# Kernel tuning notes

Measured on AMD Instinct MI355X. Metric: run time of the kernel, lower is better.

Reference implementation:

```python
import jax, jax.numpy as jnp
import numpy as np

GAMMA = 1.4
N_PTS, N_IC, HID = 32768, 16384, 128


def _mlp(layers, p):
    # tanh MLP; layers = list of (W, b), last layer linear
    h = p
    for W, b in layers[:-1]:
        h = jnp.tanh(h @ W + b)
    W, b = layers[-1]
    return h @ W + b


def setup_inputs() -> dict:
    key = jax.random.key(0)
    ks = jax.random.split(key, 16)
    d = {
        "x_train": jax.random.uniform(ks[0], (N_PTS, 3), jnp.float32),
        "x_initial": jax.random.uniform(ks[1], (N_IC, 3), jnp.float32),
        "ic": jax.random.uniform(ks[2], (4, 4), jnp.float32),
    }
    def lin(k, fi, fo):
        return jax.random.normal(k, (fi, fo), jnp.float32) * np.float32(np.sqrt(1.0 / fi))
    dims_m = [(3, HID), (HID, HID), (HID, HID), (HID, 4)]
    dims_n = [(3, HID), (HID, HID), (HID, HID), (HID, 1)]
    for i, (fi, fo) in enumerate(dims_m):
        d[f"mw{i}"] = lin(ks[3 + i], fi, fo)
        d[f"mb{i}"] = jnp.zeros((fo,), jnp.float32)
    for i, (fi, fo) in enumerate(dims_n):
        d[f"nw{i}"] = lin(ks[8 + i], fi, fo)
        d[f"nb{i}"] = jnp.zeros((fo,), jnp.float32)
    return d


def _loss(x_train, x_initial, ic,
          mw0, mb0, mw1, mb1, mw2, mb2, mw3, mb3,
          nw0, nb0, nw1, nb1, nw2, nb2, nw3, nb3):
    layers_m = [(mw0, mb0), (mw1, mb1), (mw2, mb2), (mw3, mb3)]
    layers_n = [(nw0, nb0), (nw1, nb1), (nw2, nb2), (nw3, nb3)]

    def prim(p):  # p: (3,) = (x, y, t)
        o = _mlp(layers_m, p)
        rho, pr, u, v = o[0], o[1], o[2], o[3]
        E = pr / (GAMMA - 1.0) + 0.5 * rho * (u * u + v * v)
        return rho, pr, u, v, E

    def Ufn(p):  # conserved state U1..U4
        rho, pr, u, v, E = prim(p)
        return jnp.stack([rho, rho * u, rho * v, E])

    def quant(p):  # [U1..U4, f1..f4, g1..g4]
        rho, pr, u, v, E = prim(p)
        U = jnp.stack([rho, rho * u, rho * v, E])
        f = jnp.stack([rho * u, rho * u * u + pr, rho * u * v, u * (E + pr)])
        g = jnp.stack([rho * v, rho * u * v, rho * v * v + pr, v * (E + pr)])
        return jnp.concatenate([U, f, g])

    # one fused forward-mode Jacobian sweep replaces 20 torch autograd.grad calls
    J = jax.vmap(jax.jacfwd(quant))(x_train)            # (N, 12, 3)
    Hs = jax.vmap(jax.jacfwd(jax.jacfwd(Ufn)))(x_train)  # (N, 4, 3, 3)

    mu = 0.01 * jnp.squeeze(_mlp(layers_n, x_train), -1) ** 2  # (N,)
    lap = Hs[:, :, 0, 0] + Hs[:, :, 1, 1]               # U_xx + U_yy, (N, 4)
    # res_i = U_i_t + f_i_x + g_i_y - mu * (U_i_xx + U_i_yy)
    res = J[:, 0:4, 2] + J[:, 4:8, 0] + J[:, 8:12, 1] - mu[:, None] * lap
    r = jnp.mean(res ** 2, axis=0)                      # (4,) -> r1..r4

    # initial-condition quadrant loss (masked means, jit-safe)
    pred = _mlp(layers_m, x_initial)                    # (Ni, 4)
    xl = x_initial[:, 0] < 0.5
    xr = x_initial[:, 0] > 0.5
    yt = x_initial[:, 1] > 0.5
    yb = x_initial[:, 1] < 0.5
    perm = jnp.array([0, 3, 1, 2])  # ic columns -> [rho, p, u, v] target order
    init_loss = jnp.float32(0.0)
    for row, mask in ((1, xl & yt), (3, xr & yt), (0, xl & yb), (2, xr & yb)):
        tgt = ic[row][perm]                             # (4,)
        m = mask.astype(pred.dtype)
        denom = jnp.maximum(jnp.sum(m), 1.0)
        init_loss = init_loss + jnp.sum(m[:, None] * (pred - tgt) ** 2) / denom

    return jnp.sum(r) + 10.0 * init_loss + 0.1 * jnp.mean(mu ** 2)


def reference(x_train, x_initial, ic,
              mw0, mb0, mw1, mb1, mw2, mb2, mw3, mb3,
              nw0, nb0, nw1, nb1, nw2, nb2, nw3, nb3):
    return _loss(x_train, x_initial, ic,
                 mw0, mb0, mw1, mb1, mw2, mb2, mw3, mb3,
                 nw0, nb0, nw1, nb1, nw2, nb2, nw3, nb3)
```

## Files before the change

kernel.cpp:

```cpp
#include <hip/hip_runtime.h>

#define NPTS 32768
#define NIC  16384
#define GRID 1024
#define BLK  256
#define NW   4

typedef __attribute__((ext_vector_type(8))) _Float16 f16x8;
typedef __attribute__((ext_vector_type(4))) float f32x4;

#define SWZ(e, r) ((e) ^ (((r) & 7) << 3))
#define MFMA16 __builtin_amdgcn_mfma_f32_16x16x32_f16

__device__ __forceinline__ float tanh_fast(float x) {
    float e = __expf(2.0f * x);
    return 1.0f - 2.0f / (e + 1.0f);
}

__device__ __forceinline__ float wave_allsum(float v) {
#pragma unroll
    for (int off = 32; off > 0; off >>= 1) v += __shfl_xor(v, off, 64);
    return v;
}

__device__ __forceinline__ unsigned short f2hb(float x) {
    return __builtin_bit_cast(unsigned short, (_Float16)x);
}
__device__ __forceinline__ uint2 pack4h(float a, float b, float c, float d) {
    return make_uint2((unsigned)f2hb(a) | ((unsigned)f2hb(b) << 16),
                      (unsigned)f2hb(c) | ((unsigned)f2hb(d) << 16));
}

__global__ __launch_bounds__(512) void k_prep(
    const float* __restrict__ mw1, const float* __restrict__ mw2,
    const float* __restrict__ nw1, const float* __restrict__ nw2,
    const float* __restrict__ mw3,
    unsigned short* __restrict__ wt1, unsigned short* __restrict__ wt2,
    unsigned short* __restrict__ nt1, unsigned short* __restrict__ nt2,
    unsigned short* __restrict__ w3t) {
    const int tid = threadIdx.x;
    const int bk = blockIdx.x;
    if (bk == 4) {
        for (int i = tid; i < 2048; i += 512) w3t[i] = 0;
        __syncthreads();
        if (tid < 512) {
            const int j = tid & 127, k = tid >> 7;
            w3t[k * 128 + SWZ(j, k)] = f2hb(mw3[j * 4 + k]);
        }
        return;
    }
    const float* src = (bk == 0) ? mw1 : (bk == 1) ? mw2 : (bk == 2) ? nw1 : nw2;
    unsigned short* dst = (bk == 0) ? wt1 : (bk == 1) ? wt2 : (bk == 2) ? nt1 : nt2;
    __shared__ float sM[128 * 129];
#pragma unroll
    for (int k = 0; k < 32; k++) {
        const int idx = tid + k * 512;
        const int j = idx >> 7, n = idx & 127;
        sM[n * 129 + j] = src[idx];
    }
    __syncthreads();
#pragma unroll
    for (int k = 0; k < 32; k++) {
        const int d = tid + k * 512;
        const int n = d >> 7, js = d & 127;
        const int j = js ^ ((n & 7) << 3);
        dst[d] = f2hb(sM[n * 129 + j]);
    }
}

__device__ __forceinline__ void load_aw(f16x8 (&aW)[2][4],
                                        const unsigned short* __restrict__ w,
                                        int arow0, int arow1, int g, int l15) {
#pragma unroll
    for (int ks = 0; ks < 4; ks++) {
        const int ee = SWZ(ks * 32 + g * 8, l15);
        aW[0][ks] = *(const f16x8*)&w[arow0 + ee];
        aW[1][ks] = *(const f16x8*)&w[arow1 + ee];
    }
}

template <int PT>
__device__ __forceinline__ void hidden_val(const f16x8 (&aW)[2][4], _Float16* sHv,
                                           const float* bias, int wv, int g, int l15) {
    f32x4 acc[2][PT];
#pragma unroll
    for (int rr = 0; rr < 2; rr++)
#pragma unroll
        for (int pt = 0; pt < PT; pt++) acc[rr][pt] = (f32x4){0.f, 0.f, 0.f, 0.f};
#pragma unroll
    for (int ks = 0; ks < 4; ks++) {
        const int ee = SWZ(ks * 32 + g * 8, l15);
#pragma unroll
        for (int pt = 0; pt < PT; pt++) {
            const f16x8 Bv = *(const f16x8*)&sHv[(pt * 16 + l15) * 128 + ee];
            acc[0][pt] = MFMA16(aW[0][ks], Bv, acc[0][pt], 0, 0, 0);
            acc[1][pt] = MFMA16(aW[1][ks], Bv, acc[1][pt], 0, 0, 0);
        }
    }
    __syncthreads();
    float hv[2][PT][4];
#pragma unroll
    for (int rr = 0; rr < 2; rr++)
#pragma unroll
        for (int pt = 0; pt < PT; pt++)
#pragma unroll
            for (int r = 0; r < 4; r++) {
                const int n = wv * 32 + rr * 16 + g * 4 + r;
                hv[rr][pt][r] = tanh_fast(acc[rr][pt][r] + bias[n]);
            }
#pragma unroll
    for (int rr = 0; rr < 2; rr++)
#pragma unroll
        for (int pt = 0; pt < PT; pt++) {
            const int row = pt * 16 + l15;
            *(uint2*)&sHv[row * 128 + SWZ(wv * 32 + rr * 16 + g * 4, row)] =
                pack4h(hv[rr][pt][0], hv[rr][pt][1], hv[rr][pt][2], hv[rr][pt][3]);
        }
}

__device__ __forceinline__ void hidden_res(const f16x8 (&aW)[2][4], _Float16* sH6,
                                           const float* bias, int wv, int g, int l15) {
    f32x4 acc[2][6];
#pragma unroll
    for (int rr = 0; rr < 2; rr++)
#pragma unroll
        for (int c = 0; c < 6; c++) acc[rr][c] = (f32x4){0.f, 0.f, 0.f, 0.f};
#pragma unroll
    for (int ks = 0; ks < 4; ks++) {
        const int ee = SWZ(ks * 32 + g * 8, l15);
#pragma unroll
        for (int c = 0; c < 6; c++) {
            const f16x8 Bv = *(const f16x8*)&sH6[c * 2048 + l15 * 128 + ee];
            acc[0][c] = MFMA16(aW[0][ks], Bv, acc[0][c], 0, 0, 0);
            acc[1][c] = MFMA16(aW[1][ks], Bv, acc[1][c], 0, 0, 0);
        }
    }
    __syncthreads();
    float ch[2][6][4];
#pragma unroll
    for (int rr = 0; rr < 2; rr++)
#pragma unroll
        for (int r = 0; r < 4; r++) {
            const int n = wv * 32 + rr * 16 + g * 4 + r;
            const float z0 = acc[rr][0][r] + bias[n];
            const float a = tanh_fast(z0);
            const float s = 1.f - a * a;
            const float zx = acc[rr][1][r], zy = acc[rr][2][r];
            ch[rr][0][r] = a;
            ch[rr][1][r] = s * zx;
            ch[rr][2][r] = s * zy;
            ch[rr][3][r] = s * acc[rr][3][r];
            ch[rr][4][r] = s * acc[rr][4][r] - 2.f * a * s * zx * zx;
            ch[rr][5][r] = s * acc[rr][5][r] - 2.f * a * s * zy * zy;
        }
#pragma unroll
    for (int rr = 0; rr < 2; rr++) {
        const int eo = l15 * 128 + SWZ(wv * 32 + rr * 16 + g * 4, l15);
#pragma unroll
        for (int c = 0; c < 6; c++)
            *(uint2*)&sH6[c * 2048 + eo] =
                pack4h(ch[rr][c][0], ch[rr][c][1], ch[rr][c][2], ch[rr][c][3]);
    }
}

__global__ __launch_bounds__(BLK) void k_fused(
    const float* __restrict__ xtr, const float* __restrict__ xin,
    const float* __restrict__ icg,
    const float* __restrict__ mw0, const float* __restrict__ mb0,
    const float* __restrict__ mb1, const float* __restrict__ mb2,
    const float* __restrict__ mb3,
    const float* __restrict__ nw0, const float* __restrict__ nb0,
    const float* __restrict__ nb1, const float* __restrict__ nb2,
    const float* __restrict__ nw3, const float* __restrict__ nb3,
    const unsigned short* __restrict__ wt1, const unsigned short* __restrict__ wt2,
    const unsigned short* __restrict__ nt1, const unsigned short* __restrict__ nt2,
    const unsigned short* __restrict__ w3t,
    float* __restrict__ resPart, float* __restrict__ muPart,
    float* __restrict__ icPart) {
    __shared__ __align__(16) _Float16 sH[6 * 2048];
    __shared__ __align__(16) _Float16 sA[2048];
    __shared__ __align__(16) float sW0[2][512];
    __shared__ __align__(16) float sO[384];
    __shared__ float sB[520];
    __shared__ float sMu[32];
    __shared__ float sTq[16];
    __shared__ float sRed[NW][8];

    const int tid = threadIdx.x;
    const int lane = tid & 63, wv = tid >> 6;
    const int g = lane >> 4, l15 = lane & 15;
    const int p16 = tid & 15, chunk = tid >> 4;
    const int arow0 = (wv * 32 + l15) * 128;
    const int arow1 = (wv * 32 + 16 + l15) * 128;

    f16x8 aW[2][4];
    load_aw(aW, nt1, arow0, arow1, g, l15);

    if (tid < 128) { sB[tid] = mb1[tid]; sB[260 + tid] = nb1[tid]; }
    else           { sB[tid] = mb2[tid - 128]; sB[260 + tid] = nb2[tid - 128]; }
    if (tid < 4) sB[256 + tid] = mb3[tid];
    if (tid == 4) sB[516] = nb3[0];
    if (tid < 16) {
        const int k = tid & 3, q = tid >> 2;
        const int row = (q == 0) ? 1 : ((q == 1) ? 3 : ((q == 2) ? 0 : 2));
        const int pc = (k == 0) ? 0 : ((k == 1) ? 3 : ((k == 2) ? 1 : 2));
        sTq[q * 4 + k] = icg[row * 4 + pc];
    }
    for (int i = tid; i < 512; i += BLK) {
        sW0[0][i] = (i < 384) ? nw0[i] : nb0[i - 384];
        sW0[1][i] = (i < 384) ? mw0[i] : mb0[i - 384];
    }
    for (int i = tid; i < 2048; i += BLK) sA[i] = (_Float16)0.f;
    if (tid < 128) sA[tid] = (_Float16)nw3[tid];
    __syncthreads();

    float accMu2 = 0.f;
    {
        const int pt0 = blockIdx.x * 32;
        const int ee0 = SWZ(chunk * 8, p16);
        const float* w0 = &sW0[0][0];
#pragma unroll
        for (int pp = 0; pp < 2; pp++) {
            const int p = pt0 + pp * 16 + p16;
            const float x = xtr[p * 3 + 0], y = xtr[p * 3 + 1], t = xtr[p * 3 + 2];
            float hv[8];
#pragma unroll
            for (int j = 0; j < 8; j++) {
                const int n = chunk * 8 + j;
                hv[j] = tanh_fast(fmaf(w0[n], x, fmaf(w0[128 + n], y,
                                       fmaf(w0[256 + n], t, w0[384 + n]))));
            }
            const uint2 lo = pack4h(hv[0], hv[1], hv[2], hv[3]);
            const uint2 hi = pack4h(hv[4], hv[5], hv[6], hv[7]);
            *(uint4*)&sH[(pp * 16 + p16) * 128 + ee0] = make_uint4(lo.x, lo.y, hi.x, hi.y);
        }
        __syncthreads();
        hidden_val<2>(aW, sH, &sB[260], wv, g, l15);
        load_aw(aW, nt2, arow0, arow1, g, l15);
        __syncthreads();
        hidden_val<2>(aW, sH, &sB[388], wv, g, l15);
        __syncthreads();
        if (wv < 2) {
            f32x4 a4 = (f32x4){0.f, 0.f, 0.f, 0.f};
#pragma unroll
            for (int ks = 0; ks < 4; ks++) {
                const int ee = SWZ(ks * 32 + g * 8, l15);
                const f16x8 Af = *(const f16x8*)&sA[l15 * 128 + ee];
                const f16x8 Bv = *(const f16x8*)&sH[(wv * 16 + l15) * 128 + ee];
                a4 = MFMA16(Af, Bv, a4, 0, 0, 0);
            }
            if (g == 0) {
                const float o = a4[0] + sB[516];
                const float muv = 0.01f * o * o;
                sMu[wv * 16 + l15] = muv;
                accMu2 += muv * muv;
            }
        }
        __syncthreads();
    }
    accMu2 = wave_allsum(accMu2);
    if (lane == 0) sRed[wv][0] = accMu2;
    __syncthreads();
    if (tid == 0)
        muPart[blockIdx.x] = sRed[0][0] + sRed[1][0] + sRed[2][0] + sRed[3][0];

    ((uint4*)sA)[tid] = ((const uint4*)w3t)[tid];
    load_aw(aW, wt1, arow0, arow1, g, l15);

    {
        const int pt0 = blockIdx.x * 16;
        const int ee0 = SWZ(chunk * 8, p16);
        const float* w0 = &sW0[1][0];
        {
            const int p = pt0 + p16;
            const float x = xin[p * 3 + 0], y = xin[p * 3 + 1], t = xin[p * 3 + 2];
            float hv[8];
#pragma unroll
            for (int j = 0; j < 8; j++) {
                const int n = chunk * 8 + j;
                hv[j] = tanh_fast(fmaf(w0[n], x, fmaf(w0[128 + n], y,
                                       fmaf(w0[256 + n], t, w0[384 + n]))));
            }
            const uint2 lo = pack4h(hv[0], hv[1], hv[2], hv[3]);
            const uint2 hi = pack4h(hv[4], hv[5], hv[6], hv[7]);
            *(uint4*)&sH[p16 * 128 + ee0] = make_uint4(lo.x, lo.y, hi.x, hi.y);
        }
        __syncthreads();
        hidden_val<1>(aW, sH, &sB[0], wv, g, l15);
        load_aw(aW, wt2, arow0, arow1, g, l15);
        __syncthreads();
        hidden_val<1>(aW, sH, &sB[128], wv, g, l15);
        __syncthreads();
        float qs[4] = {0, 0, 0, 0}, qc[4] = {0, 0, 0, 0};
        if (wv == 0) {
            f32x4 a4 = (f32x4){0.f, 0.f, 0.f, 0.f};
#pragma unroll
            for (int ks = 0; ks < 4; ks++) {
                const int ee = SWZ(ks * 32 + g * 8, l15);
                const f16x8 Af = *(const f16x8*)&sA[l15 * 128 + ee];
                const f16x8 Bv = *(const f16x8*)&sH[l15 * 128 + ee];
                a4 = MFMA16(Af, Bv, a4, 0, 0, 0);
            }
            if (g == 0) {
                const int p = pt0 + l15;
                const float o0 = a4[0] + sB[256];
                const float o1 = a4[1] + sB[257];
                const float o2 = a4[2] + sB[258];
                const float o3 = a4[3] + sB[259];
                const float x = xin[p * 3 + 0];
                const float y = xin[p * 3 + 1];
                int quad = -1;
                if (x < 0.5f && y > 0.5f) quad = 0;
                else if (x > 0.5f && y > 0.5f) quad = 1;
                else if (x < 0.5f && y < 0.5f) quad = 2;
                else if (x > 0.5f && y < 0.5f) quad = 3;
                if (quad >= 0) {
                    const float d0 = o0 - sTq[quad * 4 + 0];
                    const float d1 = o1 - sTq[quad * 4 + 1];
                    const float d2 = o2 - sTq[quad * 4 + 2];
                    const float d3 = o3 - sTq[quad * 4 + 3];
                    const float ss = d0 * d0 + d1 * d1 + d2 * d2 + d3 * d3;
#pragma unroll
                    for (int qq = 0; qq < 4; qq++) {
                        qs[qq] += (quad == qq) ? ss : 0.f;
                        qc[qq] += (quad == qq) ? 1.f : 0.f;
                    }
                }
            }
        }
        __syncthreads();
#pragma unroll
        for (int qq = 0; qq < 4; qq++) {
            qs[qq] = wave_allsum(qs[qq]);
            qc[qq] = wave_allsum(qc[qq]);
        }
        if (lane == 0) {
#pragma unroll
            for (int qq = 0; qq < 4; qq++) { sRed[wv][qq] = qs[qq]; sRed[wv][4 + qq] = qc[qq]; }
        }
        __syncthreads();
        if (tid == 0) {
#pragma unroll
            for (int q = 0; q < 8; q++)
                icPart[blockIdx.x * 8 + q] =
                    sRed[0][q] + sRed[1][q] + sRed[2][q] + sRed[3][q];
        }
        __syncthreads();
    }

    float racc0 = 0.f, racc1 = 0.f, racc2 = 0.f, racc3 = 0.f;
    const int base = blockIdx.x * 32;
    for (int b = 0; b < 2; b++) {
        const int pt0 = base + b * 16;
        load_aw(aW, wt1, arow0, arow1, g, l15);
        {
            const int p = pt0 + p16;
            const float x = xtr[p * 3 + 0], y = xtr[p * 3 + 1], t = xtr[p * 3 + 2];
            const float* w0 = &sW0[1][0];
            float ch[6][8];
#pragma unroll
            for (int j = 0; j < 8; j++) {
                const int n = chunk * 8 + j;
                const float wx = w0[n], wy = w0[128 + n], wz = w0[256 + n];
                const float z = fmaf(wx, x, fmaf(wy, y, fmaf(wz, t, w0[384 + n])));
                const float a = tanh_fast(z);
                const float s = 1.f - a * a;
                ch[0][j] = a;
                ch[1][j] = s * wx;
                ch[2][j] = s * wy;
                ch[3][j] = s * wz;
                ch[4][j] = -2.f * a * s * wx * wx;
                ch[5][j] = -2.f * a * s * wy * wy;
            }
            const int off = p16 * 128 + SWZ(chunk * 8, p16);
#pragma unroll
            for (int c = 0; c < 6; c++) {
                const uint2 lo = pack4h(ch[c][0], ch[c][1], ch[c][2], ch[c][3]);
                const uint2 hi = pack4h(ch[c][4], ch[c][5], ch[c][6], ch[c][7]);
                *(uint4*)&sH[c * 2048 + off] = make_uint4(lo.x, lo.y, hi.x, hi.y);
            }
        }
        __syncthreads();
        hidden_res(aW, sH, &sB[0], wv, g, l15);
        load_aw(aW, wt2, arow0, arow1, g, l15);
        __syncthreads();
        hidden_res(aW, sH, &sB[128], wv, g, l15);
        __syncthreads();
#pragma unroll
        for (int tt = 0; tt < 2; tt++) {
            const int c = wv + tt * 4;
            if (c < 6) {
                f32x4 a4 = (f32x4){0.f, 0.f, 0.f, 0.f};
#pragma unroll
                for (int ks = 0; ks < 4; ks++) {
                    const int ee = SWZ(ks * 32 + g * 8, l15);
                    const f16x8 Af = *(const f16x8*)&sA[l15 * 128 + ee];
                    const f16x8 Bf = *(const f16x8*)&sH[c * 2048 + l15 * 128 + ee];
                    a4 = MFMA16(Af, Bf, a4, 0, 0, 0);
                }
                if (g == 0) {
                    float4 o = make_float4(a4[0], a4[1], a4[2], a4[3]);
                    if (c == 0) { o.x += sB[256]; o.y += sB[257]; o.z += sB[258]; o.w += sB[259]; }
                    *(float4*)&sO[(c * 16 + l15) * 4] = o;
                }
            }
        }
        __syncthreads();
        if (wv == 0) {
            const int pp = lane & 15;
            const float m = sMu[b * 16 + pp];
            float oq[4][6];
#pragma unroll
            for (int c = 0; c < 6; c++) {
                const float4 o = *(const float4*)&sO[(c * 16 + pp) * 4];
                oq[0][c] = o.x; oq[1][c] = o.y; oq[2][c] = o.z; oq[3][c] = o.w;
            }
            const float rho = oq[0][0], rho_x = oq[0][1], rho_y = oq[0][2],
                        rho_t = oq[0][3], rho_xx = oq[0][4], rho_yy = oq[0][5];
            const float pr = oq[1][0], pr_x = oq[1][1], pr_y = oq[1][2],
                        pr_t = oq[1][3], pr_xx = oq[1][4], pr_yy = oq[1][5];
            const float u = oq[2][0], u_x = oq[2][1], u_y = oq[2][2],
                        u_t = oq[2][3], u_xx = oq[2][4], u_yy = oq[2][5];
            const float v = oq[3][0], v_x = oq[3][1], v_y = oq[3][2],
                        v_t = oq[3][3], v_xx = oq[3][4], v_yy = oq[3][5];

            const float ig1 = 2.5f;
            const float ke = 0.5f * (u * u + v * v);
            const float E = pr * ig1 + rho * ke;
            const float d_x = u * u_x + v * v_x;
            const float d_y = u * u_y + v * v_y;
            const float d_t = u * u_t + v * v_t;
            const float E_x = pr_x * ig1 + rho_x * ke + rho * d_x;
            const float E_y = pr_y * ig1 + rho_y * ke + rho * d_y;
            const float E_t = pr_t * ig1 + rho_t * ke + rho * d_t;
            const float E_xx = pr_xx * ig1 + rho_xx * ke + 2.f * rho_x * d_x +
                               rho * (u_x * u_x + u * u_xx + v_x * v_x + v * v_xx);
            const float E_yy = pr_yy * ig1 + rho_yy * ke + 2.f * rho_y * d_y +
                               rho * (u_y * u_y + u * u_yy + v_y * v_y + v * v_yy);

            const float r1 = rho_t + (rho_x * u + rho * u_x) + (rho_y * v + rho * v_y)
                           - m * (rho_xx + rho_yy);
            const float r2 = (rho_t * u + rho * u_t)
                           + (rho_x * u * u + 2.f * rho * u * u_x + pr_x)
                           + (rho_y * u * v + rho * u_y * v + rho * u * v_y)
                           - m * ((rho_xx * u + 2.f * rho_x * u_x + rho * u_xx)
                                + (rho_yy * u + 2.f * rho_y * u_y + rho * u_yy));
            const float r3 = (rho_t * v + rho * v_t)
                           + (rho_x * u * v + rho * u_x * v + rho * u * v_x)
                           + (rho_y * v * v + 2.f * rho * v * v_y + pr_y)
                           - m * ((rho_xx * v + 2.f * rho_x * v_x + rho * v_xx)
                                + (rho_yy * v + 2.f * rho_y * v_y + rho * v_yy));
            const float r4 = E_t
                           + (u_x * (E + pr) + u * (E_x + pr_x))
                           + (v_y * (E + pr) + v * (E_y + pr_y))
                           - m * (E_xx + E_yy);
            if (lane < 16) {
                racc0 += r1 * r1; racc1 += r2 * r2;
                racc2 += r3 * r3; racc3 += r4 * r4;
            }
        }
        __syncthreads();
    }

    if (wv == 0) {
        racc0 = wave_allsum(racc0);
        racc1 = wave_allsum(racc1);
        racc2 = wave_allsum(racc2);
        racc3 = wave_allsum(racc3);
        if (lane == 0) {
            resPart[blockIdx.x * 4 + 0] = racc0;
            resPart[blockIdx.x * 4 + 1] = racc1;
            resPart[blockIdx.x * 4 + 2] = racc2;
            resPart[blockIdx.x * 4 + 3] = racc3;
        }
    }
}

__global__ void k_fin(const float* __restrict__ resPart, const float* __restrict__ muPart,
                      const float* __restrict__ icPart, float* __restrict__ out) {
    const int lane = threadIdx.x;
    float r[4] = {0, 0, 0, 0};
    float m2 = 0.f;
    float qs[4] = {0, 0, 0, 0}, qc[4] = {0, 0, 0, 0};
    for (int b = lane; b < GRID; b += 64) {
#pragma unroll
        for (int i = 0; i < 4; i++) r[i] += resPart[b * 4 + i];
        m2 += muPart[b];
#pragma unroll
        for (int q = 0; q < 4; q++) {
            qs[q] += icPart[b * 8 + q];
            qc[q] += icPart[b * 8 + 4 + q];
        }
    }
#pragma unroll
    for (int i = 0; i < 4; i++) r[i] = wave_allsum(r[i]);
    m2 = wave_allsum(m2);
#pragma unroll
    for (int q = 0; q < 4; q++) { qs[q] = wave_allsum(qs[q]); qc[q] = wave_allsum(qc[q]); }
    if (lane == 0) {
        const float sumr = (r[0] + r[1] + r[2] + r[3]) / (float)NPTS;
        float init_loss = 0.f;
#pragma unroll
        for (int q = 0; q < 4; q++) init_loss += qs[q] / fmaxf(qc[q], 1.f);
        out[0] = sumr + 10.f * init_loss + 0.1f * (m2 / (float)NPTS);
    }
}

extern "C" void kernel_launch(void* const* d_in, const int* in_sizes, int n_in,
                              void* d_out, int out_size, void* d_ws, size_t ws_size,
                              hipStream_t stream) {
    const float* xtr = (const float*)d_in[0];
    const float* xin = (const float*)d_in[1];
    const float* icg = (const float*)d_in[2];
    const float* mw0 = (const float*)d_in[3];
    const float* mb0 = (const float*)d_in[4];
    const float* mw1 = (const float*)d_in[5];
    const float* mb1 = (const float*)d_in[6];
    const float* mw2 = (const float*)d_in[7];
    const float* mb2 = (const float*)d_in[8];
    const float* mw3 = (const float*)d_in[9];
    const float* mb3 = (const float*)d_in[10];
    const float* nw0 = (const float*)d_in[11];
    const float* nb0 = (const float*)d_in[12];
    const float* nw1 = (const float*)d_in[13];
    const float* nb1 = (const float*)d_in[14];
    const float* nw2 = (const float*)d_in[15];
    const float* nb2 = (const float*)d_in[16];
    const float* nw3 = (const float*)d_in[17];
    const float* nb3 = (const float*)d_in[18];

    float* wsf = (float*)d_ws;
    float* resPart = wsf;
    float* muPart = wsf + 4096;
    float* icPart = wsf + 5120;
    unsigned short* wt1 = (unsigned short*)(wsf + 13312);
    unsigned short* wt2 = wt1 + 16384;
    unsigned short* nt1 = wt2 + 16384;
    unsigned short* nt2 = nt1 + 16384;
    unsigned short* w3t = nt2 + 16384;

    k_prep<<<5, 512, 0, stream>>>(mw1, mw2, nw1, nw2, mw3, wt1, wt2, nt1, nt2, w3t);
    k_fused<<<GRID, BLK, 0, stream>>>(xtr, xin, icg,
                                      mw0, mb0, mb1, mb2, mb3,
                                      nw0, nb0, nb1, nb2, nw3, nb3,
                                      wt1, wt2, nt1, nt2, w3t,
                                      resPart, muPart, icPart);
    k_fin<<<1, 64, 0, stream>>>(resPart, muPart, icPart, (float*)d_out);
}
```

Baseline: 62.66 us.

## Split IC loss into separate blocks and fuse final reduction via atomic counter

The initial-condition forward pass moves out of every main block into 256 dedicated blocks, each handling 64 points with full 4-wave MMA use. Before, each of the 1024 blocks processed 16 IC points using only one wave. The k_fin launch is removed: the last block to finish, detected with an atomic counter reset in k_prep, performs the final reduction. This removes one kernel launch and gives better wave utilisation for the IC work, at the cost of a larger grid, some load imbalance between the two block types, and atomic/fence overhead.

```diff
diff --git a/kernel.cpp b/kernel.cpp
--- a/kernel.cpp
+++ b/kernel.cpp
@@ -2,7 +2,9 @@
 
 #define NPTS 32768
 #define NIC  16384
-#define GRID 1024
+#define GRID_MAIN 1024
+#define GRID_IC   256
+#define GRID_TOT  1280
 #define BLK  256
 #define NW   4
 
@@ -37,10 +39,11 @@
     const float* __restrict__ mw3,
     unsigned short* __restrict__ wt1, unsigned short* __restrict__ wt2,
     unsigned short* __restrict__ nt1, unsigned short* __restrict__ nt2,
-    unsigned short* __restrict__ w3t) {
+    unsigned short* __restrict__ w3t, unsigned int* __restrict__ doneCnt) {
     const int tid = threadIdx.x;
     const int bk = blockIdx.x;
     if (bk == 4) {
+        if (tid == 0) doneCnt[0] = 0u;
         for (int i = tid; i < 2048; i += 512) w3t[i] = 0;
         __syncthreads();
         if (tid < 512) {
@@ -176,7 +179,8 @@
     const unsigned short* __restrict__ nt1, const unsigned short* __restrict__ nt2,
     const unsigned short* __restrict__ w3t,
     float* __restrict__ resPart, float* __restrict__ muPart,
-    float* __restrict__ icPart) {
+    float* __restrict__ icPart, unsigned int* __restrict__ doneCnt,
+    float* __restrict__ out) {
     __shared__ __align__(16) _Float16 sH[6 * 2048];
     __shared__ __align__(16) _Float16 sA[2048];
     __shared__ __align__(16) float sW0[2][512];
@@ -185,6 +189,7 @@
     __shared__ float sMu[32];
     __shared__ float sTq[16];
     __shared__ float sRed[NW][8];
+    __shared__ int sFlag;
 
     const int tid = threadIdx.x;
     const int lane = tid & 63, wv = tid >> 6;
@@ -194,35 +199,222 @@
     const int arow1 = (wv * 32 + 16 + l15) * 128;
 
     f16x8 aW[2][4];
-    load_aw(aW, nt1, arow0, arow1, g, l15);
-
-    if (tid < 128) { sB[tid] = mb1[tid]; sB[260 + tid] = nb1[tid]; }
-    else           { sB[tid] = mb2[tid - 128]; sB[260 + tid] = nb2[tid - 128]; }
-    if (tid < 4) sB[256 + tid] = mb3[tid];
-    if (tid == 4) sB[516] = nb3[0];
-    if (tid < 16) {
-        const int k = tid & 3, q = tid >> 2;
-        const int row = (q == 0) ? 1 : ((q == 1) ? 3 : ((q == 2) ? 0 : 2));
-        const int pc = (k == 0) ? 0 : ((k == 1) ? 3 : ((k == 2) ? 1 : 2));
-        sTq[q * 4 + k] = icg[row * 4 + pc];
-    }
-    for (int i = tid; i < 512; i += BLK) {
-        sW0[0][i] = (i < 384) ? nw0[i] : nb0[i - 384];
-        sW0[1][i] = (i < 384) ? mw0[i] : mb0[i - 384];
-    }
-    for (int i = tid; i < 2048; i += BLK) sA[i] = (_Float16)0.f;
-    if (tid < 128) sA[tid] = (_Float16)nw3[tid];
-    __syncthreads();
-
-    float accMu2 = 0.f;
-    {
-        const int pt0 = blockIdx.x * 32;
+
+    if (blockIdx.x < GRID_MAIN) {
+        load_aw(aW, nt1, arow0, arow1, g, l15);
+        if (tid < 128) { sB[tid] = mb1[tid]; sB[260 + tid] = nb1[tid]; }
+        else           { sB[tid] = mb2[tid - 128]; sB[260 + tid] = nb2[tid - 128]; }
+        if (tid < 4) sB[256 + tid] = mb3[tid];
+        if (tid == 4) sB[516] = nb3[0];
+        for (int i = tid; i < 512; i += BLK) {
+            sW0[0][i] = (i < 384) ? nw0[i] : nb0[i - 384];
+            sW0[1][i] = (i < 384) ? mw0[i] : mb0[i - 384];
+        }
+        for (int i = tid; i < 2048; i += BLK) sA[i] = (_Float16)0.f;
+        if (tid < 128) sA[tid] = (_Float16)nw3[tid];
+        __syncthreads();
+
+        float accMu2 = 0.f;
+        {
+            const int pt0 = blockIdx.x * 32;
+            const int ee0 = SWZ(chunk * 8, p16);
+            const float* w0 = &sW0[0][0];
+#pragma unroll
+            for (int pp = 0; pp < 2; pp++) {
+                const int p = pt0 + pp * 16 + p16;
+                const float x = xtr[p * 3 + 0], y = xtr[p * 3 + 1], t = xtr[p * 3 + 2];
+                float hv[8];
+#pragma unroll
+                for (int j = 0; j < 8; j++) {
+                    const int n = chunk * 8 + j;
+                    hv[j] = tanh_fast(fmaf(w0[n], x, fmaf(w0[128 + n], y,
+                                           fmaf(w0[256 + n], t, w0[384 + n]))));
+                }
+                const uint2 lo = pack4h(hv[0], hv[1], hv[2], hv[3]);
+                const uint2 hi = pack4h(hv[4], hv[5], hv[6], hv[7]);
+                *(uint4*)&sH[(pp * 16 + p16) * 128 + ee0] = make_uint4(lo.x, lo.y, hi.x, hi.y);
+            }
+            __syncthreads();
+            hidden_val<2>(aW, sH, &sB[260], wv, g, l15);
+            load_aw(aW, nt2, arow0, arow1, g, l15);
+            __syncthreads();
+            hidden_val<2>(aW, sH, &sB[388], wv, g, l15);
+            __syncthreads();
+            if (wv < 2) {
+                f32x4 a4 = (f32x4){0.f, 0.f, 0.f, 0.f};
+#pragma unroll
+                for (int ks = 0; ks < 4; ks++) {
+                    const int ee = SWZ(ks * 32 + g * 8, l15);
+                    const f16x8 Af = *(const f16x8*)&sA[l15 * 128 + ee];
+                    const f16x8 Bv = *(const f16x8*)&sH[(wv * 16 + l15) * 128 + ee];
+                    a4 = MFMA16(Af, Bv, a4, 0, 0, 0);
+                }
+                if (g == 0) {
+                    const float o = a4[0] + sB[516];
+                    const float muv = 0.01f * o * o;
+                    sMu[wv * 16 + l15] = muv;
+                    accMu2 += muv * muv;
+                }
+            }
+            __syncthreads();
+        }
+        accMu2 = wave_allsum(accMu2);
+        if (lane == 0) sRed[wv][0] = accMu2;
+        __syncthreads();
+        if (tid == 0)
+            muPart[blockIdx.x] = sRed[0][0] + sRed[1][0] + sRed[2][0] + sRed[3][0];
+
+        ((uint4*)sA)[tid] = ((const uint4*)w3t)[tid];
+
+        float racc0 = 0.f, racc1 = 0.f, racc2 = 0.f, racc3 = 0.f;
+        const int base = blockIdx.x * 32;
+        for (int b = 0; b < 2; b++) {
+            const int pt0 = base + b * 16;
+            load_aw(aW, wt1, arow0, arow1, g, l15);
+            {
+                const int p = pt0 + p16;
+                const float x = xtr[p * 3 + 0], y = xtr[p * 3 + 1], t = xtr[p * 3 + 2];
+                const float* w0 = &sW0[1][0];
+                float ch[6][8];
+#pragma unroll
+                for (int j = 0; j < 8; j++) {
+                    const int n = chunk * 8 + j;
+                    const float wx = w0[n], wy = w0[128 + n], wz = w0[256 + n];
+                    const float z = fmaf(wx, x, fmaf(wy, y, fmaf(wz, t, w0[384 + n])));
+                    const float a = tanh_fast(z);
+                    const float s = 1.f - a * a;
+                    ch[0][j] = a;
+                    ch[1][j] = s * wx;
+                    ch[2][j] = s * wy;
+                    ch[3][j] = s * wz;
+                    ch[4][j] = -2.f * a * s * wx * wx;
+                    ch[5][j] = -2.f * a * s * wy * wy;
+                }
+                const int off = p16 * 128 + SWZ(chunk * 8, p16);
+#pragma unroll
+                for (int c = 0; c < 6; c++) {
+                    const uint2 lo = pack4h(ch[c][0], ch[c][1], ch[c][2], ch[c][3]);
+                    const uint2 hi = pack4h(ch[c][4], ch[c][5], ch[c][6], ch[c][7]);
+                    *(uint4*)&sH[c * 2048 + off] = make_uint4(lo.x, lo.y, hi.x, hi.y);
+                }
+            }
+            __syncthreads();
+            hidden_res(aW, sH, &sB[0], wv, g, l15);
+            load_aw(aW, wt2, arow0, arow1, g, l15);
+            __syncthreads();
+            hidden_res(aW, sH, &sB[128], wv, g, l15);
+            __syncthreads();
+#pragma unroll
+            for (int tt = 0; tt < 2; tt++) {
+                const int c = wv + tt * 4;
+                if (c < 6) {
+                    f32x4 a4 = (f32x4){0.f, 0.f, 0.f, 0.f};
+#pragma unroll
+                    for (int ks = 0; ks < 4; ks++) {
+                        const int ee = SWZ(ks * 32 + g * 8, l15);
+                        const f16x8 Af = *(const f16x8*)&sA[l15 * 128 + ee];
+                        const f16x8 Bf = *(const f16x8*)&sH[c * 2048 + l15 * 128 + ee];
+                        a4 = MFMA16(Af, Bf, a4, 0, 0, 0);
+                    }
+                    if (g == 0) {
+                        float4 o = make_float4(a4[0], a4[1], a4[2], a4[3]);
+                        if (c == 0) { o.x += sB[256]; o.y += sB[257]; o.z += sB[258]; o.w += sB[259]; }
+                        *(float4*)&sO[(c * 16 + l15) * 4] = o;
+                    }
+                }
+            }
+            __syncthreads();
+            if (wv == 0) {
+                const int pp = lane & 15;
+                const float m = sMu[b * 16 + pp];
+                float oq[4][6];
+#pragma unroll
+                for (int c = 0; c < 6; c++) {
+                    const float4 o = *(const float4*)&sO[(c * 16 + pp) * 4];
+                    oq[0][c] = o.x; oq[1][c] = o.y; oq[2][c] = o.z; oq[3][c] = o.w;
+                }
+                const float rho = oq[0][0], rho_x = oq[0][1], rho_y = oq[0][2],
+                            rho_t = oq[0][3], rho_xx = oq[0][4], rho_yy = oq[0][5];
+                const float pr = oq[1][0], pr_x = oq[1][1], pr_y = oq[1][2],
+                            pr_t = oq[1][3], pr_xx = oq[1][4], pr_yy = oq[1][5];
+                const float u = oq[2][0], u_x = oq[2][1], u_y = oq[2][2],
+                            u_t = oq[2][3], u_xx = oq[2][4], u_yy = oq[2][5];
+                const float v = oq[3][0], v_x = oq[3][1], v_y = oq[3][2],
+                            v_t = oq[3][3], v_xx = oq[3][4], v_yy = oq[3][5];
+
+                const float ig1 = 2.5f;
+                const float ke = 0.5f * (u * u + v * v);
+                const float E = pr * ig1 + rho * ke;
+                const float d_x = u * u_x + v * v_x;
+                const float d_y = u * u_y + v * v_y;
+                const float d_t = u * u_t + v * v_t;
+                const float E_x = pr_x * ig1 + rho_x * ke + rho * d_x;
+                const float E_y = pr_y * ig1 + rho_y * ke + rho * d_y;
+                const float E_t = pr_t * ig1 + rho_t * ke + rho * d_t;
+                const float E_xx = pr_xx * ig1 + rho_xx * ke + 2.f * rho_x * d_x +
+                                   rho * (u_x * u_x + u * u_xx + v_x * v_x + v * v_xx);
+                const float E_yy = pr_yy * ig1 + rho_yy * ke + 2.f * rho_y * d_y +
+                                   rho * (u_y * u_y + u * u_yy + v_y * v_y + v * v_yy);
+
+                const float r1 = rho_t + (rho_x * u + rho * u_x) + (rho_y * v + rho * v_y)
+                               - m * (rho_xx + rho_yy);
+                const float r2 = (rho_t * u + rho * u_t)
+                               + (rho_x * u * u + 2.f * rho * u * u_x + pr_x)
+                               + (rho_y * u * v + rho * u_y * v + rho * u * v_y)
+                               - m * ((rho_xx * u + 2.f * rho_x * u_x + rho * u_xx)
+                                    + (rho_yy * u + 2.f * rho_y * u_y + rho * u_yy));
+                const float r3 = (rho_t * v + rho * v_t)
+                               + (rho_x * u * v + rho * u_x * v + rho * u * v_x)
+                               + (rho_y * v * v + 2.f * rho * v * v_y + pr_y)
+                               - m * ((rho_xx * v + 2.f * rho_x * v_x + rho * v_xx)
+                                    + (rho_yy * v + 2.f * rho_y * v_y + rho * v_yy));
+                const float r4 = E_t
+                               + (u_x * (E + pr) + u * (E_x + pr_x))
+                               + (v_y * (E + pr) + v * (E_y + pr_y))
+                               - m * (E_xx + E_yy);
+                if (lane < 16) {
+                    racc0 += r1 * r1; racc1 += r2 * r2;
+                    racc2 += r3 * r3; racc3 += r4 * r4;
+                }
+            }
+            __syncthreads();
+        }
+        if (wv == 0) {
+            racc0 = wave_allsum(racc0);
+            racc1 = wave_allsum(racc1);
+            racc2 = wave_allsum(racc2);
+            racc3 = wave_allsum(racc3);
+            if (lane == 0) {
+                resPart[blockIdx.x * 4 + 0] = racc0;
+                resPart[blockIdx.x * 4 + 1] = racc1;
+                resPart[blockIdx.x * 4 + 2] = racc2;
+                resPart[blockIdx.x * 4 + 3] = racc3;
+            }
+        }
+    } else {
+        const int bid2 = blockIdx.x - GRID_MAIN;
+        load_aw(aW, wt1, arow0, arow1, g, l15);
+        if (tid < 128) { sB[tid] = mb1[tid]; }
+        else           { sB[tid] = mb2[tid - 128]; }
+        if (tid < 4) sB[256 + tid] = mb3[tid];
+        if (tid < 16) {
+            const int k = tid & 3, q = tid >> 2;
+            const int row = (q == 0) ? 1 : ((q == 1) ? 3 : ((q == 2) ? 0 : 2));
+            const int pc = (k == 0) ? 0 : ((k == 1) ? 3 : ((k == 2) ? 1 : 2));
+            sTq[q * 4 + k] = icg[row * 4 + pc];
+        }
+        for (int i = tid; i < 512; i += BLK)
+            sW0[1][i] = (i < 384) ? mw0[i] : mb0[i - 384];
+        ((uint4*)sA)[tid] = ((const uint4*)w3t)[tid];
+        __syncthreads();
+
+        const int pt0 = bid2 * 64;
         const int ee0 = SWZ(chunk * 8, p16);
-        const float* w0 = &sW0[0][0];
-#pragma unroll
-        for (int pp = 0; pp < 2; pp++) {
+        const float* w0 = &sW0[1][0];
+#pragma unroll
+        for (int pp = 0; pp < 4; pp++) {
             const int p = pt0 + pp * 16 + p16;
-            const float x = xtr[p * 3 + 0], y = xtr[p * 3 + 1], t = xtr[p * 3 + 2];
+            const float x = xin[p * 3 + 0], y = xin[p * 3 + 1], t = xin[p * 3 + 2];
             float hv[8];
 #pragma unroll
             for (int j = 0; j < 8; j++) {
@@ -235,12 +427,13 @@
             *(uint4*)&sH[(pp * 16 + p16) * 128 + ee0] = make_uint4(lo.x, lo.y, hi.x, hi.y);
         }
         __syncthreads();
-        hidden_val<2>(aW, sH, &sB[260], wv, g, l15);
-        load_aw(aW, nt2, arow0, arow1, g, l15);
-        __syncthreads();
-        hidden_val<2>(aW, sH, &sB[388], wv, g, l15);
-        __syncthreads();
-        if (wv < 2) {
+        hidden_val<4>(aW, sH, &sB[0], wv, g, l15);
+        load_aw(aW, wt2, arow0, arow1, g, l15);
+        __syncthreads();
+        hidden_val<4>(aW, sH, &sB[128], wv, g, l15);
+        __syncthreads();
+        float qs[4] = {0, 0, 0, 0}, qc[4] = {0, 0, 0, 0};
+        {
             f32x4 a4 = (f32x4){0.f, 0.f, 0.f, 0.f};
 #pragma unroll
             for (int ks = 0; ks < 4; ks++) {
@@ -250,59 +443,7 @@
                 a4 = MFMA16(Af, Bv, a4, 0, 0, 0);
             }
             if (g == 0) {
-                const float o = a4[0] + sB[516];
-                const float muv = 0.01f * o * o;
-                sMu[wv * 16 + l15] = muv;
-                accMu2 += muv * muv;
-            }
-        }
-        __syncthreads();
-    }
-    accMu2 = wave_allsum(accMu2);
-    if (lane == 0) sRed[wv][0] = accMu2;
-    __syncthreads();
-    if (tid == 0)
-        muPart[blockIdx.x] = sRed[0][0] + sRed[1][0] + sRed[2][0] + sRed[3][0];
-
-    ((uint4*)sA)[tid] = ((const uint4*)w3t)[tid];
-    load_aw(aW, wt1, arow0, arow1, g, l15);
-
-    {
-        const int pt0 = blockIdx.x * 16;
-        const int ee0 = SWZ(chunk * 8, p16);
-        const float* w0 = &sW0[1][0];
-        {
-            const int p = pt0 + p16;
-            const float x = xin[p * 3 + 0], y = xin[p * 3 + 1], t = xin[p * 3 + 2];
-            float hv[8];
-#pragma unroll
-            for (int j = 0; j < 8; j++) {
-                const int n = chunk * 8 + j;
-                hv[j] = tanh_fast(fmaf(w0[n], x, fmaf(w0[128 + n], y,
-                                       fmaf(w0[256 + n], t, w0[384 + n]))));
-            }
-            const uint2 lo = pack4h(hv[0], hv[1], hv[2], hv[3]);
-            const uint2 hi = pack4h(hv[4], hv[5], hv[6], hv[7]);
-            *(uint4*)&sH[p16 * 128 + ee0] = make_uint4(lo.x, lo.y, hi.x, hi.y);
-        }
-        __syncthreads();
-        hidden_val<1>(aW, sH, &sB[0], wv, g, l15);
-        load_aw(aW, wt2, arow0, arow1, g, l15);
-        __syncthreads();
-        hidden_val<1>(aW, sH, &sB[128], wv, g, l15);
-        __syncthreads();
-        float qs[4] = {0, 0, 0, 0}, qc[4] = {0, 0, 0, 0};
-        if (wv == 0) {
-            f32x4 a4 = (f32x4){0.f, 0.f, 0.f, 0.f};
-#pragma unroll
-            for (int ks = 0; ks < 4; ks++) {
-                const int ee = SWZ(ks * 32 + g * 8, l15);
-                const f16x8 Af = *(const f16x8*)&sA[l15 * 128 + ee];
-                const f16x8 Bv = *(const f16x8*)&sH[l15 * 128 + ee];
-                a4 = MFMA16(Af, Bv, a4, 0, 0, 0);
-            }
-            if (g == 0) {
-                const int p = pt0 + l15;
+                const int p = pt0 + wv * 16 + l15;
                 const float o0 = a4[0] + sB[256];
                 const float o1 = a4[1] + sB[257];
                 const float o2 = a4[2] + sB[258];
@@ -328,7 +469,6 @@
                 }
             }
         }
-        __syncthreads();
 #pragma unroll
         for (int qq = 0; qq < 4; qq++) {
             qs[qq] = wave_allsum(qs[qq]);
@@ -342,167 +482,46 @@
         if (tid == 0) {
 #pragma unroll
             for (int q = 0; q < 8; q++)
-                icPart[blockIdx.x * 8 + q] =
+                icPart[bid2 * 8 + q] =
                     sRed[0][q] + sRed[1][q] + sRed[2][q] + sRed[3][q];
         }
-        __syncthreads();
-    }
-
-    float racc0 = 0.f, racc1 = 0.f, racc2 = 0.f, racc3 = 0.f;
-    const int base = blockIdx.x * 32;
-    for (int b = 0; b < 2; b++) {
-        const int pt0 = base + b * 16;
-        load_aw(aW, wt1, arow0, arow1, g, l15);
-        {
-            const int p = pt0 + p16;
-            const float x = xtr[p * 3 + 0], y = xtr[p * 3 + 1], t = xtr[p * 3 + 2];
-            const float* w0 = &sW0[1][0];
-            float ch[6][8];
-#pragma unroll
-            for (int j = 0; j < 8; j++) {
-                const int n = chunk * 8 + j;
-                const float wx = w0[n], wy = w0[128 + n], wz = w0[256 + n];
-                const float z = fmaf(wx, x, fmaf(wy, y, fmaf(wz, t, w0[384 + n])));
-                const float a = tanh_fast(z);
-                const float s = 1.f - a * a;
-                ch[0][j] = a;
-                ch[1][j] = s * wx;
-                ch[2][j] = s * wy;
-                ch[3][j] = s * wz;
-                ch[4][j] = -2.f * a * s * wx * wx;
-                ch[5][j] = -2.f * a * s * wy * wy;
-            }
-            const int off = p16 * 128 + SWZ(chunk * 8, p16);
-#pragma unroll
-            for (int c = 0; c < 6; c++) {
-                const uint2 lo = pack4h(ch[c][0], ch[c][1], ch[c][2], ch[c][3]);
-                const uint2 hi = pack4h(ch[c][4], ch[c][5], ch[c][6], ch[c][7]);
-                *(uint4*)&sH[c * 2048 + off] = make_uint4(lo.x, lo.y, hi.x, hi.y);
-            }
-        }
-        __syncthreads();
-        hidden_res(aW, sH, &sB[0], wv, g, l15);
-        load_aw(aW, wt2, arow0, arow1, g, l15);
-        __syncthreads();
-        hidden_res(aW, sH, &sB[128], wv, g, l15);
-        __syncthreads();
-#pragma unroll
-        for (int tt = 0; tt < 2; tt++) {
-            const int c = wv + tt * 4;
-            if (c < 6) {
-                f32x4 a4 = (f32x4){0.f, 0.f, 0.f, 0.f};
-#pragma unroll
-                for (int ks = 0; ks < 4; ks++) {
-                    const int ee = SWZ(ks * 32 + g * 8, l15);
-                    const f16x8 Af = *(const f16x8*)&sA[l15 * 128 + ee];
-                    const f16x8 Bf = *(const f16x8*)&sH[c * 2048 + l15 * 128 + ee];
-                    a4 = MFMA16(Af, Bf, a4, 0, 0, 0);
-                }
-                if (g == 0) {
-                    float4 o = make_float4(a4[0], a4[1], a4[2], a4[3]);
-                    if (c == 0) { o.x += sB[256]; o.y += sB[257]; o.z += sB[258]; o.w += sB[259]; }
-                    *(float4*)&sO[(c * 16 + l15) * 4] = o;
-                }
-            }
-        }
-        __syncthreads();
-        if (wv == 0) {
-            const int pp = lane & 15;
-            const float m = sMu[b * 16 + pp];
-            float oq[4][6];
-#pragma unroll
-            for (int c = 0; c < 6; c++) {
-                const float4 o = *(const float4*)&sO[(c * 16 + pp) * 4];
-                oq[0][c] = o.x; oq[1][c] = o.y; oq[2][c] = o.z; oq[3][c] = o.w;
-            }
-            const float rho = oq[0][0], rho_x = oq[0][1], rho_y = oq[0][2],
-                        rho_t = oq[0][3], rho_xx = oq[0][4], rho_yy = oq[0][5];
-            const float pr = oq[1][0], pr_x = oq[1][1], pr_y = oq[1][2],
-                        pr_t = oq[1][3], pr_xx = oq[1][4], pr_yy = oq[1][5];
-            const float u = oq[2][0], u_x = oq[2][1], u_y = oq[2][2],
-                        u_t = oq[2][3], u_xx = oq[2][4], u_yy = oq[2][5];
-            const float v = oq[3][0], v_x = oq[3][1], v_y = oq[3][2],
-                        v_t = oq[3][3], v_xx = oq[3][4], v_yy = oq[3][5];
-
-            const float ig1 = 2.5f;
-            const float ke = 0.5f * (u * u + v * v);
-            const float E = pr * ig1 + rho * ke;
-            const float d_x = u * u_x + v * v_x;
-            const float d_y = u * u_y + v * v_y;
-            const float d_t = u * u_t + v * v_t;
-            const float E_x = pr_x * ig1 + rho_x * ke + rho * d_x;
-            const float E_y = pr_y * ig1 + rho_y * ke + rho * d_y;
-            const float E_t = pr_t * ig1 + rho_t * ke + rho * d_t;
-            const float E_xx = pr_xx * ig1 + rho_xx * ke + 2.f * rho_x * d_x +
-                               rho * (u_x * u_x + u * u_xx + v_x * v_x + v * v_xx);
-            const float E_yy = pr_yy * ig1 + rho_yy * ke + 2.f * rho_y * d_y +
-                               rho * (u_y * u_y + u * u_yy + v_y * v_y + v * v_yy);
-
-            const float r1 = rho_t + (rho_x * u + rho * u_x) + (rho_y * v + rho * v_y)
-                           - m * (rho_xx + rho_yy);
-            const float r2 = (rho_t * u + rho * u_t)
-                           + (rho_x * u * u + 2.f * rho * u * u_x + pr_x)
-                           + (rho_y * u * v + rho * u_y * v + rho * u * v_y)
-                           - m * ((rho_xx * u + 2.f * rho_x * u_x + rho * u_xx)
-                                + (rho_yy * u + 2.f * rho_y * u_y + rho * u_yy));
-            const float r3 = (rho_t * v + rho * v_t)
-                           + (rho_x * u * v + rho * u_x * v + rho * u * v_x)
-                           + (rho_y * v * v + 2.f * rho * v * v_y + pr_y)
-                           - m * ((rho_xx * v + 2.f * rho_x * v_x + rho * v_xx)
-                                + (rho_yy * v + 2.f * rho_y * v_y + rho * v_yy));
-            const float r4 = E_t
-                           + (u_x * (E + pr) + u * (E_x + pr_x))
-                           + (v_y * (E + pr) + v * (E_y + pr_y))
-                           - m * (E_xx + E_yy);
-            if (lane < 16) {
-                racc0 += r1 * r1; racc1 += r2 * r2;
-                racc2 += r3 * r3; racc3 += r4 * r4;
-            }
-        }
-        __syncthreads();
-    }
-
-    if (wv == 0) {
-        racc0 = wave_allsum(racc0);
-        racc1 = wave_allsum(racc1);
-        racc2 = wave_allsum(racc2);
-        racc3 = wave_allsum(racc3);
-        if (lane == 0) {
-            resPart[blockIdx.x * 4 + 0] = racc0;
-            resPart[blockIdx.x * 4 + 1] = racc1;
-            resPart[blockIdx.x * 4 + 2] = racc2;
-            resPart[blockIdx.x * 4 + 3] = racc3;
-        }
-    }
-}
-
-__global__ void k_fin(const float* __restrict__ resPart, const float* __restrict__ muPart,
-                      const float* __restrict__ icPart, float* __restrict__ out) {
-    const int lane = threadIdx.x;
-    float r[4] = {0, 0, 0, 0};
-    float m2 = 0.f;
-    float qs[4] = {0, 0, 0, 0}, qc[4] = {0, 0, 0, 0};
-    for (int b = lane; b < GRID; b += 64) {
-#pragma unroll
-        for (int i = 0; i < 4; i++) r[i] += resPart[b * 4 + i];
-        m2 += muPart[b];
-#pragma unroll
-        for (int q = 0; q < 4; q++) {
-            qs[q] += icPart[b * 8 + q];
-            qc[q] += icPart[b * 8 + 4 + q];
-        }
-    }
-#pragma unroll
-    for (int i = 0; i < 4; i++) r[i] = wave_allsum(r[i]);
-    m2 = wave_allsum(m2);
-#pragma unroll
-    for (int q = 0; q < 4; q++) { qs[q] = wave_allsum(qs[q]); qc[q] = wave_allsum(qc[q]); }
-    if (lane == 0) {
-        const float sumr = (r[0] + r[1] + r[2] + r[3]) / (float)NPTS;
-        float init_loss = 0.f;
-#pragma unroll
-        for (int q = 0; q < 4; q++) init_loss += qs[q] / fmaxf(qc[q], 1.f);
-        out[0] = sumr + 10.f * init_loss + 0.1f * (m2 / (float)NPTS);
+    }
+
+    if (tid == 0) {
+        __threadfence();
+        const unsigned old = atomicAdd(doneCnt, 1u);
+        sFlag = (old == GRID_TOT - 1) ? 1 : 0;
+    }
+    __syncthreads();
+    if (sFlag && tid < 64) {
+        __threadfence();
+        float r[4] = {0, 0, 0, 0};
+        float m2 = 0.f;
+        float fqs[4] = {0, 0, 0, 0}, fqc[4] = {0, 0, 0, 0};
+        for (int b = tid; b < GRID_MAIN; b += 64) {
+#pragma unroll
+            for (int i = 0; i < 4; i++) r[i] += resPart[b * 4 + i];
+            m2 += muPart[b];
+        }
+        for (int b = tid; b < GRID_IC; b += 64) {
+#pragma unroll
+            for (int q = 0; q < 4; q++) {
+                fqs[q] += icPart[b * 8 + q];
+                fqc[q] += icPart[b * 8 + 4 + q];
+            }
+        }
+#pragma unroll
+        for (int i = 0; i < 4; i++) r[i] = wave_allsum(r[i]);
+        m2 = wave_allsum(m2);
+#pragma unroll
+        for (int q = 0; q < 4; q++) { fqs[q] = wave_allsum(fqs[q]); fqc[q] = wave_allsum(fqc[q]); }
+        if (tid == 0) {
+            const float sumr = (r[0] + r[1] + r[2] + r[3]) / (float)NPTS;
+            float init_loss = 0.f;
+#pragma unroll
+            for (int q = 0; q < 4; q++) init_loss += fqs[q] / fmaxf(fqc[q], 1.f);
+            out[0] = sumr + 10.f * init_loss + 0.1f * (m2 / (float)NPTS);
+        }
     }
 }
 
@@ -533,17 +552,18 @@
     float* resPart = wsf;
     float* muPart = wsf + 4096;
     float* icPart = wsf + 5120;
+    unsigned int* doneCnt = (unsigned int*)(wsf + 7168);
     unsigned short* wt1 = (unsigned short*)(wsf + 13312);
     unsigned short* wt2 = wt1 + 16384;
     unsigned short* nt1 = wt2 + 16384;
     unsigned short* nt2 = nt1 + 16384;
     unsigned short* w3t = nt2 + 16384;
 
-    k_prep<<<5, 512, 0, stream>>>(mw1, mw2, nw1, nw2, mw3, wt1, wt2, nt1, nt2, w3t);
-    k_fused<<<GRID, BLK, 0, stream>>>(xtr, xin, icg,
-                                      mw0, mb0, mb1, mb2, mb3,
-                                      nw0, nb0, nb1, nb2, nw3, nb3,
-                                      wt1, wt2, nt1, nt2, w3t,
-                                      resPart, muPart, icPart);
-    k_fin<<<1, 64, 0, stream>>>(resPart, muPart, icPart, (float*)d_out);
-}
+    k_prep<<<5, 512, 0, stream>>>(mw1, mw2, nw1, nw2, mw3, wt1, wt2, nt1, nt2, w3t, doneCnt);
+    k_fused<<<GRID_TOT, BLK, 0, stream>>>(xtr, xin, icg,
+                                          mw0, mb0, mb1, mb2, mb3,
+                                          nw0, nb0, nb1, nb2, nw3, nb3,
+                                          wt1, wt2, nt1, nt2, w3t,
+                                          resPart, muPart, icPart, doneCnt,
+                                          (float*)d_out);
+}
```

Measured after the change: 99.10 us. +58.1%, slower.
